# Optimization experiments

Hardware: AMD Instinct MI355X
Metric: run time of the kernel (lower is better)

Reference implementation:

```python
import jax, jax.numpy as jnp
import numpy as np

B, H, W, C = 32, 56, 56, 192
WS, SHIFT, HEADS = 7, 3, 6
HEAD_DIM = C // HEADS
SCALE = 0.17677669529663687  # 1/sqrt(32), passed as qk_scale
HIDDEN = 4 * C
N = WS * WS
EPS = 1e-3


def _rel_index(ws):
    coords = np.stack(np.meshgrid(np.arange(ws), np.arange(ws), indexing='ij')).reshape(2, -1)
    rel = (coords[:, :, None] - coords[:, None, :]).transpose(1, 2, 0)
    rel[:, :, 0] += ws - 1
    rel[:, :, 1] += ws - 1
    rel[:, :, 0] *= 2 * ws - 1
    return rel.sum(-1)  # [N, N] int


def _attn_mask(h, w, ws, ss):
    img = np.zeros((h, w), np.float32)
    cnt = 0
    for hs in (slice(0, -ws), slice(-ws, -ss), slice(-ss, None)):
        for wsl in (slice(0, -ws), slice(-ws, -ss), slice(-ss, None)):
            img[hs, wsl] = cnt
            cnt += 1
    win = img.reshape(h // ws, ws, w // ws, ws).transpose(0, 2, 1, 3).reshape(-1, ws * ws)
    diff = win[:, None, :] - win[:, :, None]
    return np.where(diff != 0, -100.0, 0.0).astype(np.float32)  # [nW, N, N]


REL_IDX = jnp.asarray(_rel_index(WS).reshape(-1))          # [N*N]
ATTN_MASK = jnp.asarray(_attn_mask(H, W, WS, SHIFT))       # [nW, N, N]
NW = ATTN_MASK.shape[0]


def _window_partition(x, ws):
    b, h, w, c = x.shape
    x = x.reshape(b, h // ws, ws, w // ws, ws, c).transpose(0, 1, 3, 2, 4, 5)
    return x.reshape(-1, ws, ws, c)


def _window_reverse(x, ws, h, w):
    c = x.shape[-1]
    x = x.reshape(-1, h // ws, w // ws, ws, ws, c).transpose(0, 1, 3, 2, 4, 5)
    return x.reshape(-1, h, w, c)


def _layer_norm(x, g, b):
    mu = jnp.mean(x, axis=-1, keepdims=True)
    var = jnp.var(x, axis=-1, keepdims=True)
    return (x - mu) * jax.lax.rsqrt(var + EPS) * g + b


def _forward(x, ln1_g, ln1_b, w_qkv, b_qkv, bias_table, w_proj, b_proj,
             ln2_g, ln2_b, w_ffn1, bn1_scale, bn1_shift, w_ffn2, bn2_scale, bn2_shift):
    shortcut = x
    h = _layer_norm(x, ln1_g, ln1_b)
    h = jnp.roll(h, (-SHIFT, -SHIFT), axis=(1, 2))
    xw = _window_partition(h, WS).reshape(-1, N, C)  # [B*nW, N, C]

    qkv = xw @ w_qkv + b_qkv                          # [B*nW, N, 3C]
    qkv = qkv.reshape(-1, N, 3, HEADS, HEAD_DIM).transpose(2, 0, 3, 1, 4)
    q, k, v = qkv[0] * SCALE, qkv[1], qkv[2]          # [B*nW, heads, N, hd]

    attn = jnp.einsum('whnd,whmd->whnm', q, k)        # [B*nW, heads, N, N]
    rel_bias = bias_table[REL_IDX].reshape(N, N, HEADS).transpose(2, 0, 1)
    attn = attn + rel_bias[None]
    attn = attn.reshape(-1, NW, HEADS, N, N) + ATTN_MASK[None, :, None]
    attn = jax.nn.softmax(attn.reshape(-1, HEADS, N, N), axis=-1)

    o = jnp.einsum('whnm,whmd->whnd', attn, v)        # [B*nW, heads, N, hd]
    o = o.transpose(0, 2, 1, 3).reshape(-1, N, C)
    o = o @ w_proj + b_proj

    o = _window_reverse(o.reshape(-1, WS, WS, C), WS, H, W)
    o = jnp.roll(o, (SHIFT, SHIFT), axis=(1, 2))
    x = shortcut + o

    y = _layer_norm(x, ln2_g, ln2_b)
    dn = ('NHWC', 'HWIO', 'NHWC')
    y = jax.lax.conv_general_dilated(y, w_ffn1, (1, 1), 'SAME', dimension_numbers=dn)
    y = y * bn1_scale + bn1_shift
    y = jax.nn.gelu(y, approximate=False)
    y = jax.lax.conv_general_dilated(y, w_ffn2, (1, 1), 'SAME', dimension_numbers=dn)
    y = y * bn2_scale + bn2_shift
    return x + y


def setup_inputs() -> dict:
    key = jax.random.key(0)
    ks = jax.random.split(key, 8)
    s = lambda n: 0.02
    return {
        'x': jax.random.normal(ks[0], (B, H, W, C), jnp.float32),
        'ln1_g': jnp.ones((C,), jnp.float32),
        'ln1_b': jnp.zeros((C,), jnp.float32),
        'w_qkv': jax.random.normal(ks[1], (C, 3 * C), jnp.float32) * (C ** -0.5),
        'b_qkv': jnp.zeros((3 * C,), jnp.float32),
        'bias_table': jax.random.truncated_normal(ks[2], -2.0, 2.0, ((2 * WS - 1) ** 2, HEADS), jnp.float32) * 0.02,
        'w_proj': jax.random.normal(ks[3], (C, C), jnp.float32) * (C ** -0.5),
        'b_proj': jnp.zeros((C,), jnp.float32),
        'ln2_g': jnp.ones((C,), jnp.float32),
        'ln2_b': jnp.zeros((C,), jnp.float32),
        'w_ffn1': jax.random.normal(ks[4], (3, 3, C, HIDDEN), jnp.float32) * ((9 * C) ** -0.5),
        'bn1_scale': jnp.ones((HIDDEN,), jnp.float32),
        'bn1_shift': jnp.zeros((HIDDEN,), jnp.float32),
        'w_ffn2': jax.random.normal(ks[5], (1, 1, HIDDEN, C), jnp.float32) * (HIDDEN ** -0.5),
        'bn2_scale': jnp.ones((C,), jnp.float32),
        'bn2_shift': jnp.zeros((C,), jnp.float32),
    }


def reference(x, ln1_g, ln1_b, w_qkv, b_qkv, bias_table, w_proj, b_proj,
              ln2_g, ln2_b, w_ffn1, bn1_scale, bn1_shift, w_ffn2, bn2_scale, bn2_shift):
    return _forward(x, ln1_g, ln1_b, w_qkv, b_qkv, bias_table, w_proj, b_proj,
                    ln2_g, ln2_b, w_ffn1, bn1_scale, bn1_shift, w_ffn2, bn2_scale, bn2_shift)
```

## Files before the change

### kernel.cpp

```cpp
#include <hip/hip_runtime.h>
#include <hip/hip_bf16.h>
#include <math.h>

#define DEVINL __device__ __forceinline__

typedef __bf16 bf16x8 __attribute__((ext_vector_type(8)));
typedef float  f32x4  __attribute__((ext_vector_type(4)));

DEVINL float bf2f(unsigned short h){ return __builtin_bit_cast(float, (unsigned)h << 16); }
DEVINL unsigned short f2bf(float f){
  unsigned u = __builtin_bit_cast(unsigned, f);
  u += 0x7fffu + ((u >> 16) & 1u);
  return (unsigned short)(u >> 16);
}

DEVINL void gl16(const unsigned short* g, unsigned short* l){
  __builtin_amdgcn_global_load_lds((const __attribute__((address_space(1))) unsigned int*)g,
                                   (__attribute__((address_space(3))) unsigned int*)l,
                                   16, 0, 0);
}

#define Bn 32
#define Hn 56
#define Wn 56
#define Cn 192
#define WSz 7
#define SHIFTn 3
#define HEADSn 6
#define HDn 32
#define NWIN 49
#define NPIX (Bn*Hn*Wn)
#define HIDDENn 768
#define KCONV (9*Cn)
#define PADH 58
#define QKSCALE 0.17677669529663687f

DEVINL float wave_sum(float v){
  #pragma unroll
  for (int off=32; off; off>>=1) v += __shfl_xor(v, off, 64);
  return v;
}

__global__ __launch_bounds__(256) void k_ln1(const float* __restrict__ x,
                                             const float* __restrict__ g,
                                             const float* __restrict__ bb,
                                             unsigned short* __restrict__ h)
{
  int row  = blockIdx.x*4 + (threadIdx.x >> 6);
  int lane = threadIdx.x & 63;
  int win = row / NWIN, n = row % NWIN;
  int b = win >> 6, rem = win & 63, wh = rem >> 3, ww = rem & 7;
  int i = n / WSz, j = n % WSz;
  int rr = (wh*WSz + i + SHIFTn) % Hn;
  int cc = (ww*WSz + j + SHIFTn) % Wn;
  const float* xr = x + (size_t)((b*Hn + rr)*Wn + cc)*Cn;
  float v0 = xr[lane], v1 = xr[lane+64], v2 = xr[lane+128];
  float s  = wave_sum(v0+v1+v2);
  float sq = wave_sum(v0*v0+v1*v1+v2*v2);
  float mu = s * (1.0f/Cn);
  float var = sq * (1.0f/Cn) - mu*mu;
  float rs = rsqrtf(var + 1e-3f);
  unsigned short* hr = h + (size_t)row*Cn;
  hr[lane]     = f2bf((v0-mu)*rs*g[lane]     + bb[lane]);
  hr[lane+64]  = f2bf((v1-mu)*rs*g[lane+64]  + bb[lane+64]);
  hr[lane+128] = f2bf((v2-mu)*rs*g[lane+128] + bb[lane+128]);
}

__global__ __launch_bounds__(256) void k_ln2(const float* __restrict__ xmid,
                                             const float* __restrict__ g,
                                             const float* __restrict__ bb,
                                             unsigned short* __restrict__ out)
{
  int p    = blockIdx.x*4 + (threadIdx.x >> 6);
  int lane = threadIdx.x & 63;
  int b = p / (Hn*Wn), rc = p % (Hn*Wn);
  int r = rc / Wn, c = rc % Wn;
  const float* xr = xmid + (size_t)p*Cn;
  float v0 = xr[lane], v1 = xr[lane+64], v2 = xr[lane+128];
  float s  = wave_sum(v0+v1+v2);
  float sq = wave_sum(v0*v0+v1*v1+v2*v2);
  float mu = s * (1.0f/Cn);
  float var = sq * (1.0f/Cn) - mu*mu;
  float rs = rsqrtf(var + 1e-3f);
  unsigned short* orow = out + (size_t)((b*PADH + r + 1)*PADH + (c + 1))*Cn;
  orow[lane]     = f2bf((v0-mu)*rs*g[lane]     + bb[lane]);
  orow[lane+64]  = f2bf((v1-mu)*rs*g[lane+64]  + bb[lane+64]);
  orow[lane+128] = f2bf((v2-mu)*rs*g[lane+128] + bb[lane+128]);
}

__global__ __launch_bounds__(256) void k_transpose(const float* __restrict__ in,
                                                   unsigned short* __restrict__ out,
                                                   int K, int N)
{
  int idx = blockIdx.x*256 + threadIdx.x;
  if (idx < K*N){ int k = idx / N, n = idx - k*N; out[(size_t)n*K + k] = f2bf(in[idx]); }
}

__global__ __launch_bounds__(256) void k_attn(const unsigned short* __restrict__ qkv,
                                              const float* __restrict__ bias_table,
                                              unsigned short* __restrict__ o,
                                              int win_base)
{
  __shared__ float qs[NWIN][HDn], ks[NWIN][HDn], vs[NWIN][HDn], S[NWIN][NWIN+1];
  int head = blockIdx.x, lwin = blockIdx.y;
  int gwin = win_base + lwin;
  int tid = threadIdx.x;
  const unsigned short* base = qkv + (size_t)lwin*NWIN*576 + head*HDn;
  for (int t = tid; t < NWIN*HDn; t += 256){
    int n = t >> 5, d = t & 31;
    const unsigned short* rp = base + (size_t)n*576 + d;
    qs[n][d] = bf2f(rp[0]) * QKSCALE;
    ks[n][d] = bf2f(rp[192]);
    vs[n][d] = bf2f(rp[384]);
  }
  __syncthreads();
  int rem = gwin & 63, wh = rem >> 3, ww = rem & 7;
  for (int t = tid; t < NWIN*NWIN; t += 256){
    int p = t / NWIN, q = t - p*NWIN;
    float acc = 0.f;
    #pragma unroll
    for (int d = 0; d < HDn; ++d) acc += qs[p][d]*ks[q][d];
    int pi = p/7, pj = p%7, qi = q/7, qj = q%7;
    int rel = (pi-qi+6)*13 + (pj-qj+6);
    acc += bias_table[rel*HEADSn + head];
    int pr = wh*7+pi, pc = ww*7+pj, qr = wh*7+qi, qc = ww*7+qj;
    int cp = (pr<49?0:(pr<53?1:2))*3 + (pc<49?0:(pc<53?1:2));
    int cq = (qr<49?0:(qr<53?1:2))*3 + (qc<49?0:(qc<53?1:2));
    if (cp != cq) acc -= 100.0f;
    S[p][q] = acc;
  }
  __syncthreads();
  if (tid < NWIN){
    float m = -1e30f;
    for (int q=0;q<NWIN;++q) m = fmaxf(m, S[tid][q]);
    float sum = 0.f;
    for (int q=0;q<NWIN;++q){ float e = expf(S[tid][q]-m); S[tid][q]=e; sum+=e; }
    float inv = 1.0f/sum;
    for (int q=0;q<NWIN;++q) S[tid][q] *= inv;
  }
  __syncthreads();
  for (int t = tid; t < NWIN*HDn; t += 256){
    int n = t >> 5, d = t & 31;
    float acc = 0.f;
    for (int m=0;m<NWIN;++m) acc += S[n][m]*vs[m][d];
    o[((size_t)gwin*NWIN + n)*Cn + head*HDn + d] = f2bf(acc);
  }
}

template<int AMODE, int EPI, int BMt, int BNt>
__global__ __launch_bounds__(256) void k_gemm(const unsigned short* __restrict__ A,
                                              const unsigned short* __restrict__ Bt,
                                              int K, int a_rbase, int o_rbase,
                                              const float* __restrict__ e0,
                                              const float* __restrict__ e1,
                                              const float* __restrict__ e2,
                                              void* __restrict__ out)
{
  constexpr int WMT = BMt/32, WNT = BNt/32;
  constexpr int NIA = BMt/64, NIB = BNt/64;
  __shared__ __align__(16) unsigned short As[BMt*32];
  __shared__ __align__(16) unsigned short Bs[BNt*32];
  int tid = threadIdx.x;
  int bm = blockIdx.y * BMt, bn = blockIdx.x * BNt;
  int wave = tid >> 6, lane = tid & 63;
  int l15 = lane & 15, quad = lane >> 4;
  int wm = (wave & 1) * (BMt/2), wn = (wave >> 1) * (BNt/2);

  int srow = tid >> 2;
  int kc   = (tid & 3) * 8;

  size_t abase[NIA];
  #pragma unroll
  for (int i=0;i<NIA;++i){
    int lrow = bm + i*64 + srow;
    if (AMODE == 0) abase[i] = (size_t)(a_rbase + lrow) * K + kc;
    else {
      int grow = a_rbase + lrow;
      int b = grow / (Hn*Wn), rc = grow % (Hn*Wn);
      int r = rc / Wn, c = rc - r*Wn;
      abase[i] = (size_t)((b*PADH + r)*PADH + c) * Cn + kc;
    }
  }
  size_t bbase[NIB];
  #pragma unroll
  for (int i=0;i<NIB;++i) bbase[i] = (size_t)(bn + i*64 + srow) * K + kc;

  f32x4 acc[WMT][WNT] = {};

  int nkb = K / 32;
  for (int kb = 0; kb < nkb; ++kb){
    int k0 = kb * 32;
    size_t aoff;
    if (AMODE == 0) aoff = (size_t)k0;
    else {
      int tap = k0 / Cn, ci = k0 - tap*Cn;
      int dh = tap/3, dw = tap - dh*3;
      aoff = (size_t)((dh*PADH + dw)*Cn + ci);
    }
    #pragma unroll
    for (int i=0;i<NIA;++i)
      gl16(A + abase[i] + aoff, &As[i*64*32] + (size_t)tid*8);
    #pragma unroll
    for (int i=0;i<NIB;++i)
      gl16(Bt + bbase[i] + (size_t)k0, &Bs[i*64*32] + (size_t)tid*8);
    __syncthreads();

    bf16x8 af[WMT], bfr[WNT];
    #pragma unroll
    for (int mt=0;mt<WMT;++mt) af[mt]  = *(const bf16x8*)&As[(wm + mt*16 + l15)*32 + quad*8];
    #pragma unroll
    for (int nt=0;nt<WNT;++nt) bfr[nt] = *(const bf16x8*)&Bs[(wn + nt*16 + l15)*32 + quad*8];
    #pragma unroll
    for (int mt=0;mt<WMT;++mt)
      #pragma unroll
      for (int nt=0;nt<WNT;++nt)
        acc[mt][nt] = __builtin_amdgcn_mfma_f32_16x16x32_bf16(af[mt], bfr[nt], acc[mt][nt], 0,0,0);
    __syncthreads();
  }

  #pragma unroll
  for (int mt=0; mt<WMT; ++mt)
  #pragma unroll
  for (int nt=0; nt<WNT; ++nt){
    f32x4 a4 = acc[mt][nt];
    int gcol = bn + wn + nt*16 + l15;
    #pragma unroll
    for (int r=0; r<4; ++r){
      int orow = bm + wm + mt*16 + quad*4 + r;
      float v = a4[r];
      if (EPI == 0){
        v += e0[gcol];
        ((unsigned short*)out)[(size_t)orow*576 + gcol] = f2bf(v);
      } else if (EPI == 1){
        v += e0[gcol];
        int grow = o_rbase + orow;
        int win = grow / NWIN, n = grow - win*NWIN;
        int b = win >> 6, rem2 = win & 63, wh = rem2 >> 3, ww = rem2 & 7;
        int ii = n / WSz, jj = n - ii*WSz;
        int fr = (wh*WSz + ii + SHIFTn) % Hn;
        int fc = (ww*WSz + jj + SHIFTn) % Wn;
        size_t idx = (size_t)((b*Hn + fr)*Wn + fc)*Cn + gcol;
        ((float*)out)[idx] = e2[idx] + v;
      } else if (EPI == 2){
        v = v * e0[gcol] + e1[gcol];
        v = 0.5f * v * (1.0f + erff(v * 0.7071067811865476f));
        ((unsigned short*)out)[(size_t)orow*HIDDENn + gcol] = f2bf(v);
      } else {
        v = v * e0[gcol] + e1[gcol];
        int grow = o_rbase + orow;
        v += e2[(size_t)grow*Cn + gcol];
        ((float*)out)[(size_t)grow*Cn + gcol] = v;
      }
    }
  }
}

extern "C" void kernel_launch(void* const* d_in, const int* in_sizes, int n_in,
                              void* d_out, int out_size, void* d_ws, size_t ws_size,
                              hipStream_t stream)
{
  const float* x        = (const float*)d_in[0];
  const float* ln1_g    = (const float*)d_in[1];
  const float* ln1_b    = (const float*)d_in[2];
  const float* w_qkv    = (const float*)d_in[3];
  const float* b_qkv    = (const float*)d_in[4];
  const float* btab     = (const float*)d_in[5];
  const float* w_proj   = (const float*)d_in[6];
  const float* b_proj   = (const float*)d_in[7];
  const float* ln2_g    = (const float*)d_in[8];
  const float* ln2_b    = (const float*)d_in[9];
  const float* w_ffn1   = (const float*)d_in[10];
  const float* bn1_s    = (const float*)d_in[11];
  const float* bn1_sh   = (const float*)d_in[12];
  const float* w_ffn2   = (const float*)d_in[13];
  const float* bn2_s    = (const float*)d_in[14];
  const float* bn2_sh   = (const float*)d_in[15];

  const size_t szA   = 41337344;
  const size_t xmsz  = (size_t)NPIX*Cn*4;
  const size_t wtsz  = 221184 + 73728 + 2654208 + 294912;
  int nch = 8;
  for (int cand = 1; cand <= 8; cand <<= 1){
    size_t need = szA + ((size_t)NPIX*HIDDENn*2)/cand + xmsz + wtsz + (1u<<20);
    if (need <= ws_size){ nch = cand; break; }
  }
  const int mc = NPIX / nch;
  const int wc = 2048 / nch;

  char* ws = (char*)d_ws;
  size_t off = 0;
  unsigned short* h      = (unsigned short*)(ws + off);
  unsigned short* ln2pad = (unsigned short*)(ws + off);  off += szA;
  unsigned short* qc     = (unsigned short*)(ws + off);
  unsigned short* hc     = (unsigned short*)(ws + off);  off += ((size_t)NPIX*HIDDENn*2)/nch;
  float*          xmid   = (float*)(ws + off);           off += xmsz;
  unsigned short* wTq    = (unsigned short*)(ws + off);  off += 221184;
  unsigned short* wTp    = (unsigned short*)(ws + off);  off += 73728;
  unsigned short* wTf1   = (unsigned short*)(ws + off);  off += 2654208;
  unsigned short* wTf2   = (unsigned short*)(ws + off);
  float*          outp   = (float*)d_out;
  unsigned short* obuf   = (unsigned short*)d_out;

  dim3 blk(256);

  k_transpose<<<(192*576 + 255)/256,  blk, 0, stream>>>(w_qkv,  wTq,  192, 576);
  k_transpose<<<(192*192 + 255)/256,  blk, 0, stream>>>(w_proj, wTp,  192, 192);
  k_transpose<<<(1728*768 + 255)/256, blk, 0, stream>>>(w_ffn1, wTf1, 1728, 768);
  k_transpose<<<(768*192 + 255)/256,  blk, 0, stream>>>(w_ffn2, wTf2, 768, 192);

  k_ln1<<<NPIX/4, blk, 0, stream>>>(x, ln1_g, ln1_b, h);

  for (int c = 0; c < nch; ++c){
    int rbase = c * mc;
    k_gemm<0,0,128,64><<<dim3(576/64, mc/128), blk, 0, stream>>>(
        h, wTq, 192, rbase, 0, b_qkv, nullptr, nullptr, qc);
    k_attn<<<dim3(HEADSn, wc), blk, 0, stream>>>(qc, btab, obuf, c*wc);
  }

  k_gemm<0,1,128,64><<<dim3(192/64, NPIX/128), blk, 0, stream>>>(
      obuf, wTp, 192, 0, 0, b_proj, nullptr, x, xmid);

  hipMemsetAsync(ln2pad, 0, (size_t)Bn*PADH*PADH*Cn*2, stream);
  k_ln2<<<NPIX/4, blk, 0, stream>>>(xmid, ln2_g, ln2_b, ln2pad);

  for (int c = 0; c < nch; ++c){
    int rbase = c * mc;
    if (nch <= 4)
      k_gemm<1,2,128,128><<<dim3(HIDDENn/128, mc/128), blk, 0, stream>>>(
          ln2pad, wTf1, KCONV, rbase, 0, bn1_s, bn1_sh, nullptr, hc);
    else
      k_gemm<1,2,128,64><<<dim3(HIDDENn/64, mc/128), blk, 0, stream>>>(
          ln2pad, wTf1, KCONV, rbase, 0, bn1_s, bn1_sh, nullptr, hc);
    k_gemm<0,3,128,64><<<dim3(192/64, mc/128), blk, 0, stream>>>(
        hc, wTf2, 768, 0, rbase, bn2_s, bn2_sh, xmid, outp);
  }
}
```

Measured before the change: 1.148 ms.

## Add 256x256 eight-wave implicit-GEMM conv kernel with interleaved prefetch for FFN1

Replaces the generic 128-tile implicit-GEMM for the 3x3 FFN1 convolution with a dedicated 512-thread kernel that computes 256x256 output tiles. It double-buffers the LDS loads, splits each K-step into four MFMA phases with the next tile's global-to-LDS loads interleaved, and raises wave priority around the MFMA blocks. The goal is more data reuse per tile and better overlap of memory and matrix work in the dominant GEMM. In exchange it uses large LDS buffers and high register pressure at one block per CU, and it assumes mc is divisible by 256.

After: 1.066 ms. 7.1% less time.

```diff
diff --git a/kernel.cpp b/kernel.cpp
--- a/kernel.cpp
+++ b/kernel.cpp
@@ -255,6 +255,164 @@
   }
 }
 
+__global__ __launch_bounds__(512, 1) void k_gemm8conv(
+    const unsigned short* __restrict__ A,
+    const unsigned short* __restrict__ Bt,
+    int a_rbase,
+    const float* __restrict__ e0,
+    const float* __restrict__ e1,
+    unsigned short* __restrict__ out)
+{
+  __shared__ __align__(16) unsigned short As[2*256*64];
+  __shared__ __align__(16) unsigned short Bs[2*256*64];
+  const int tid  = threadIdx.x;
+  const int wave = tid >> 6, lane = tid & 63;
+  const int l15  = lane & 15, quad = lane >> 4;
+  const int wm   = (wave & 1) * 128;
+  const int wn   = (wave >> 1) * 64;
+  const int bm   = blockIdx.y * 256, bn = blockIdx.x * 256;
+
+  const int srow = tid >> 3;
+  const int scs  = (tid & 7) ^ (srow & 7);
+  const int ldst = tid * 8;
+
+  size_t abase[4], bbase[4];
+  #pragma unroll
+  for (int i=0;i<4;++i){
+    int grow = a_rbase + bm + i*64 + srow;
+    int b = grow / (Hn*Wn), rc = grow % (Hn*Wn);
+    int r = rc / Wn, c = rc - r*Wn;
+    abase[i] = (size_t)((b*PADH + r)*PADH + c)*Cn + scs*8;
+    bbase[i] = (size_t)(bn + i*64 + srow)*KCONV + scs*8;
+  }
+
+  const int cx0 = ((quad    ) ^ (l15 & 7)) * 8;
+  const int cx1 = ((quad + 4) ^ (l15 & 7)) * 8;
+
+  f32x4 acc[8][4] = {};
+  bf16x8 af[4][2], bfr[4][2];
+
+  const int ntot = KCONV/64;
+
+  #pragma unroll
+  for (int i=0;i<4;++i) gl16(Bt + bbase[i],      Bs + i*4096 + ldst);
+  #pragma unroll
+  for (int i=0;i<4;++i) gl16(A  + abase[i],      As + i*4096 + ldst);
+  #pragma unroll
+  for (int i=0;i<4;++i) gl16(Bt + bbase[i] + 64, Bs + 16384 + i*4096 + ldst);
+  #pragma unroll
+  for (int i=0;i<4;++i) gl16(A  + abase[i] + 64, As + 16384 + i*4096 + ldst);
+  asm volatile("s_waitcnt vmcnt(8)" ::: "memory");
+  __builtin_amdgcn_s_barrier();
+
+  for (int t = 0; t < ntot; ++t){
+    const unsigned short* Ac = As + (t&1)*16384;
+    const unsigned short* Bc = Bs + (t&1)*16384;
+    unsigned short* Asn = As + (t&1)*16384;
+    unsigned short* Bsn = Bs + (t&1)*16384;
+    const bool pf = (t+2 < ntot);
+    const int t2 = t + 2;
+    const int tap2 = t2/3;
+    const int dh2 = tap2/3, dw2 = tap2 - dh2*3, ci2 = (t2 - tap2*3)*64;
+    const size_t aoff2 = (size_t)(dh2*PADH + dw2)*Cn + ci2;
+    const size_t boff2 = (size_t)t2*64;
+
+    #pragma unroll
+    for (int mt=0; mt<4; ++mt){
+      const unsigned short* rp = Ac + (wm + mt*16 + l15)*64;
+      af[mt][0] = *(const bf16x8*)(rp + cx0);
+      af[mt][1] = *(const bf16x8*)(rp + cx1);
+    }
+    #pragma unroll
+    for (int nn=0; nn<4; ++nn){
+      const unsigned short* rp = Bc + (wn + nn*16 + l15)*64;
+      bfr[nn][0] = *(const bf16x8*)(rp + cx0);
+      bfr[nn][1] = *(const bf16x8*)(rp + cx1);
+    }
+    asm volatile("s_waitcnt lgkmcnt(0)" ::: "memory");
+    __builtin_amdgcn_sched_barrier(0);
+    __builtin_amdgcn_s_barrier();
+    if (pf){ gl16(Bt + bbase[0] + boff2, Bsn + 0*4096 + ldst);
+             gl16(Bt + bbase[1] + boff2, Bsn + 1*4096 + ldst); }
+    __builtin_amdgcn_s_setprio(1);
+    #pragma unroll
+    for (int mt=0; mt<4; ++mt)
+      #pragma unroll
+      for (int nn=0; nn<2; ++nn)
+        #pragma unroll
+        for (int kk=0; kk<2; ++kk)
+          acc[mt][nn] = __builtin_amdgcn_mfma_f32_16x16x32_bf16(af[mt][kk], bfr[nn][kk], acc[mt][nn], 0,0,0);
+    __builtin_amdgcn_s_setprio(0);
+    __builtin_amdgcn_s_barrier();
+
+    if (pf){ gl16(Bt + bbase[2] + boff2, Bsn + 2*4096 + ldst);
+             gl16(Bt + bbase[3] + boff2, Bsn + 3*4096 + ldst); }
+    __builtin_amdgcn_s_setprio(1);
+    #pragma unroll
+    for (int mt=0; mt<4; ++mt)
+      #pragma unroll
+      for (int nn=2; nn<4; ++nn)
+        #pragma unroll
+        for (int kk=0; kk<2; ++kk)
+          acc[mt][nn] = __builtin_amdgcn_mfma_f32_16x16x32_bf16(af[mt][kk], bfr[nn][kk], acc[mt][nn], 0,0,0);
+    __builtin_amdgcn_s_setprio(0);
+    __builtin_amdgcn_s_barrier();
+
+    #pragma unroll
+    for (int mt=0; mt<4; ++mt){
+      const unsigned short* rp = Ac + (wm + 64 + mt*16 + l15)*64;
+      af[mt][0] = *(const bf16x8*)(rp + cx0);
+      af[mt][1] = *(const bf16x8*)(rp + cx1);
+    }
+    asm volatile("s_waitcnt lgkmcnt(0)" ::: "memory");
+    __builtin_amdgcn_sched_barrier(0);
+    __builtin_amdgcn_s_barrier();
+    if (pf){ gl16(A + abase[0] + aoff2, Asn + 0*4096 + ldst);
+             gl16(A + abase[1] + aoff2, Asn + 1*4096 + ldst); }
+    __builtin_amdgcn_s_setprio(1);
+    #pragma unroll
+    for (int mt=0; mt<4; ++mt)
+      #pragma unroll
+      for (int nn=0; nn<2; ++nn)
+        #pragma unroll
+        for (int kk=0; kk<2; ++kk)
+          acc[4+mt][nn] = __builtin_amdgcn_mfma_f32_16x16x32_bf16(af[mt][kk], bfr[nn][kk], acc[4+mt][nn], 0,0,0);
+    __builtin_amdgcn_s_setprio(0);
+    __builtin_amdgcn_s_barrier();
+
+    if (pf){ gl16(A + abase[2] + aoff2, Asn + 2*4096 + ldst);
+             gl16(A + abase[3] + aoff2, Asn + 3*4096 + ldst); }
+    __builtin_amdgcn_s_setprio(1);
+    #pragma unroll
+    for (int mt=0; mt<4; ++mt)
+      #pragma unroll
+      for (int nn=2; nn<4; ++nn)
+        #pragma unroll
+        for (int kk=0; kk<2; ++kk)
+          acc[4+mt][nn] = __builtin_amdgcn_mfma_f32_16x16x32_bf16(af[mt][kk], bfr[nn][kk], acc[4+mt][nn], 0,0,0);
+    __builtin_amdgcn_s_setprio(0);
+    if (pf)                  { asm volatile("s_waitcnt vmcnt(8)" ::: "memory"); }
+    else if (t+1 < ntot)     { asm volatile("s_waitcnt vmcnt(0)" ::: "memory"); }
+    __builtin_amdgcn_s_barrier();
+  }
+
+  const int orow0 = bm + wm + quad*4;
+  #pragma unroll
+  for (int nn=0; nn<4; ++nn){
+    int gcol = bn + wn + nn*16 + l15;
+    float s0 = e0[gcol], s1 = e1[gcol];
+    #pragma unroll
+    for (int mt=0; mt<8; ++mt){
+      #pragma unroll
+      for (int r=0; r<4; ++r){
+        float v = acc[mt][nn][r] * s0 + s1;
+        v = 0.5f * v * (1.0f + erff(v * 0.7071067811865476f));
+        out[(size_t)(orow0 + mt*16 + r)*HIDDENn + gcol] = f2bf(v);
+      }
+    }
+  }
+}
+
 extern "C" void kernel_launch(void* const* d_in, const int* in_sizes, int n_in,
                               void* d_out, int out_size, void* d_ws, size_t ws_size,
                               hipStream_t stream)
@@ -325,12 +483,8 @@
 
   for (int c = 0; c < nch; ++c){
     int rbase = c * mc;
-    if (nch <= 4)
-      k_gemm<1,2,128,128><<<dim3(HIDDENn/128, mc/128), blk, 0, stream>>>(
-          ln2pad, wTf1, KCONV, rbase, 0, bn1_s, bn1_sh, nullptr, hc);
-    else
-      k_gemm<1,2,128,64><<<dim3(HIDDENn/64, mc/128), blk, 0, stream>>>(
-          ln2pad, wTf1, KCONV, rbase, 0, bn1_s, bn1_sh, nullptr, hc);
+    k_gemm8conv<<<dim3(HIDDENn/256, mc/256), dim3(512), 0, stream>>>(
+        ln2pad, wTf1, rbase, bn1_s, bn1_sh, hc);
     k_gemm<0,3,128,64><<<dim3(192/64, mc/128), blk, 0, stream>>>(
         hc, wTf2, 768, 0, rbase, bn2_s, bn2_sh, xmid, outp);
   }
```
